# Optimization experiments

Hardware: AMD Instinct MI355X
Metric: run time of the kernel (lower is better)

The kernel has to match this reference:

```python
import jax, jax.numpy as jnp
import numpy as np

N_NODES = 100000
N_EDGES = 1600000
IN_DIM, HID_DIM, OUT_DIM = 128, 256, 512
BN_EPS = 1e-5


def setup_inputs() -> dict:
    key = jax.random.key(0)
    ks = jax.random.split(key, 10)
    x = jax.random.normal(ks[0], (N_NODES, IN_DIM), dtype=jnp.float32)
    edge_index = jax.random.randint(ks[1], (2, N_EDGES), 0, N_NODES, dtype=jnp.int64)
    def lin(k, o, i):
        return jax.random.normal(k, (o, i), dtype=jnp.float32) * (1.0 / np.sqrt(i))
    return {
        "x": x,
        "edge_index": edge_index,
        # SAGEConv 1: in_dim -> hidden_dim (lin_l has bias, lin_r has none)
        "W1l": lin(ks[2], HID_DIM, IN_DIM),
        "b1": jnp.zeros((HID_DIM,), dtype=jnp.float32),
        "W1r": lin(ks[3], HID_DIM, IN_DIM),
        # BatchNorm1d(hidden_dim)
        "gamma": jnp.ones((HID_DIM,), dtype=jnp.float32),
        "beta": jnp.zeros((HID_DIM,), dtype=jnp.float32),
        # SAGEConv 2: hidden_dim -> gnn_out_dim
        "W2l": lin(ks[4], OUT_DIM, HID_DIM),
        "b2": jnp.zeros((OUT_DIM,), dtype=jnp.float32),
        "W2r": lin(ks[5], OUT_DIM, HID_DIM),
    }


def _sage_max(h, src, dst, Wl, b, Wr, n_nodes):
    # gather source features, max-aggregate onto destination nodes
    agg = jax.ops.segment_max(h[src], dst, num_segments=n_nodes)  # [N, D]
    agg = jnp.where(jnp.isneginf(agg), 0.0, agg)  # PyG fills empty segments with 0
    return agg @ Wl.T + b + h @ Wr.T


def reference(x, edge_index, W1l, b1, W1r, gamma, beta, W2l, b2, W2r):
    src, dst = edge_index[0], edge_index[1]
    n = x.shape[0]
    # layer 1: SAGEConv(in_dim, hidden_dim, aggr='max')
    h = _sage_max(x, src, dst, W1l, b1, W1r, n)
    # BatchNorm1d (batch statistics), Dropout is identity in eval; no activation in 'sage' branch
    mean = jnp.mean(h, axis=0)
    var = jnp.var(h, axis=0)
    h = gamma * (h - mean) * jax.lax.rsqrt(var + BN_EPS) + beta
    # layer 2: SAGEConv(hidden_dim, gnn_out_dim, aggr='max')
    out = _sage_max(h, src, dst, W2l, b2, W2r, n)
    return out
```

## Files before the change

### kernel.cpp

```cpp
#include <hip/hip_runtime.h>
#include <hip/hip_bf16.h>
#include <stdint.h>

#define N_NODES 100000
#define N_EDGES 1600000
#define IN_DIM 128
#define HID_DIM 256
#define OUT_DIM 512
#define NBUK 391
#define BCAP 8192
#define EPB 4096

typedef __attribute__((ext_vector_type(4))) float f32x4;
typedef __attribute__((ext_vector_type(8))) short bf16x8;

__device__ __forceinline__ float bf16lo(uint32_t u){ uint32_t b = u << 16; return __builtin_bit_cast(float, b); }
__device__ __forceinline__ float bf16hi(uint32_t u){ uint32_t b = u & 0xffff0000u; return __builtin_bit_cast(float, b); }
__device__ __forceinline__ uint16_t f32_to_bf16(float f){
  uint32_t u = __builtin_bit_cast(uint32_t, f);
  uint32_t r = (u + 0x7fffu + ((u >> 16) & 1u)) >> 16;
  return (uint16_t)r;
}
__device__ __forceinline__ uint32_t pack_bf16_exact(float lo, float hi){
  return (__builtin_bit_cast(uint32_t, hi) & 0xffff0000u) | (__builtin_bit_cast(uint32_t, lo) >> 16);
}
__device__ __forceinline__ uint32_t pack_bf16_rne(float lo, float hi){
  return (uint32_t)f32_to_bf16(lo) | ((uint32_t)f32_to_bf16(hi) << 16);
}
__device__ __forceinline__ void gl2lds16(const void* g, void* l){
  __builtin_amdgcn_global_load_lds(
      (const __attribute__((address_space(1))) uint32_t*)g,
      (__attribute__((address_space(3))) uint32_t*)l, 16, 0, 0);
}

__global__ void k_init(int* __restrict__ gcur, float* __restrict__ sum,
                       float* __restrict__ sumsq){
  int t = threadIdx.x;
  if (t < NBUK) gcur[t] = t << 13;
  if (t < 256){ sum[t] = 0.f; sumsq[t] = 0.f; }
}

__global__ void k_bucket(const int* __restrict__ src, const int* __restrict__ dst,
                         int* __restrict__ gcur, int* __restrict__ ebuk){
  __shared__ int hist[NBUK], curs[NBUK], base[NBUK];
  const int tid = threadIdx.x;
  const int e0 = blockIdx.x * EPB;
  for (int t = tid; t < NBUK; t += 256) hist[t] = 0;
  __syncthreads();
  for (int i = 0; i < EPB; i += 256){
    int e = e0 + i + tid;
    if (e < N_EDGES) atomicAdd(&hist[dst[e] >> 8], 1);
  }
  __syncthreads();
  for (int t = tid; t < NBUK; t += 256){
    int h = hist[t];
    base[t] = h ? atomicAdd(&gcur[t], h) : 0;
    curs[t] = 0;
  }
  __syncthreads();
  for (int i = 0; i < EPB; i += 256){
    int e = e0 + i + tid;
    if (e < N_EDGES){
      int d = dst[e];
      int b = d >> 8;
      int idx = atomicAdd(&curs[b], 1);
      int pos = base[b] + idx;
      if (pos < ((b + 1) << 13))
        ebuk[pos] = ((d & 255) << 17) | src[e];
    }
  }
}

__global__ void k_s2(const int* __restrict__ gcur, int* __restrict__ barr,
                     int* __restrict__ row_start){
  __shared__ int wtot[8];
  const int tid = threadIdx.x, lane = tid & 63, wv = tid >> 6;
  const int val = (tid < NBUK) ? (gcur[tid] - (tid << 13)) : 0;
  int v = val;
  #pragma unroll
  for (int d = 1; d < 64; d <<= 1){ int t = __shfl_up(v, d); if (lane >= d) v += t; }
  if (lane == 63) wtot[wv] = v;
  __syncthreads();
  if (tid < 8){
    int t = wtot[tid];
    #pragma unroll
    for (int d = 1; d < 8; d <<= 1){ int u = __shfl_up(t, d); if (tid >= d) t += u; }
    wtot[tid] = t;
  }
  __syncthreads();
  int excl = (wv ? wtot[wv - 1] : 0) + (v - val);
  if (tid <= NBUK) barr[tid] = excl;
  if (tid == 0) row_start[N_NODES] = N_EDGES;
}

__global__ __launch_bounds__(256)
void k_fillc(const int* __restrict__ gcur, const int* __restrict__ barr,
             const int* __restrict__ ebuk, int* __restrict__ row_start,
             int* __restrict__ esrc){
  __shared__ int ebuf[BCAP];
  __shared__ int cnt[256];
  __shared__ int wtot[4];
  const int b = blockIdx.x, tid = threadIdx.x, lane = tid & 63, wv = tid >> 6;
  const int nodebase = b << 8;
  const int nodecnt = min(256, N_NODES - nodebase);
  int size_b = gcur[b] - (b << 13);
  if (size_b > BCAP) size_b = BCAP;
  const int bs = barr[b];
  cnt[tid] = 0;
  for (int i = tid; i < size_b; i += 256) ebuf[i] = ebuk[(b << 13) + i];
  __syncthreads();
  for (int i = tid; i < size_b; i += 256) atomicAdd(&cnt[ebuf[i] >> 17], 1);
  __syncthreads();
  const int c = cnt[tid];
  int v = c;
  #pragma unroll
  for (int d = 1; d < 64; d <<= 1){ int t = __shfl_up(v, d); if (lane >= d) v += t; }
  if (lane == 63) wtot[wv] = v;
  __syncthreads();
  if (tid < 4){
    int t = wtot[tid];
    #pragma unroll
    for (int d = 1; d < 4; d <<= 1){ int u = __shfl_up(t, d); if (tid >= d) t += u; }
    wtot[tid] = t;
  }
  __syncthreads();
  const int excl = (wv ? wtot[wv - 1] : 0) + (v - c);
  if (tid < nodecnt) row_start[nodebase + tid] = bs + excl;
  cnt[tid] = excl;
  __syncthreads();
  for (int i = tid; i < size_b; i += 256){
    int p = ebuf[i];
    int pos = atomicAdd(&cnt[p >> 17], 1);
    esrc[bs + pos] = p & 0x1FFFF;
  }
}

__global__ void k_convx(const float* __restrict__ x, uint16_t* __restrict__ A1){
  const int idx = blockIdx.x * 256 + threadIdx.x;
  const int n = idx >> 5, q = idx & 31;
  const float4 v = *(const float4*)(x + (long)n * 128 + q * 4);
  ushort4 o;
  o.x = f32_to_bf16(v.x); o.y = f32_to_bf16(v.y);
  o.z = f32_to_bf16(v.z); o.w = f32_to_bf16(v.w);
  *(ushort4*)(A1 + (long)n * 256 + 128 + q * 4) = o;
}

__global__ void k_w1(const float* __restrict__ W1l, const float* __restrict__ W1r,
                     uint16_t* __restrict__ W1cat){
  int idx = blockIdx.x * 256 + threadIdx.x;
  int j = idx >> 8, k = idx & 255;
  float v = (k < 128) ? W1l[j * 128 + k] : W1r[j * 128 + (k - 128)];
  W1cat[idx] = f32_to_bf16(v);
}

__global__ void k_w2(const float* __restrict__ W2l, const float* __restrict__ W2r,
                     const float* __restrict__ b2, const float* __restrict__ scale,
                     const float* __restrict__ shift, uint16_t* __restrict__ W2cat,
                     float* __restrict__ bias2){
  const int wid = (blockIdx.x * 256 + threadIdx.x) >> 6;
  const int lane = threadIdx.x & 63;
  if (wid >= OUT_DIM) return;
  float part = 0.f;
  #pragma unroll
  for (int t = 0; t < 4; t++){
    int k = t * 64 + lane;
    float wl = W2l[(long)wid * 256 + k];
    W2cat[(long)wid * 512 + k] = f32_to_bf16(wl);
    float wr = W2r[(long)wid * 256 + k];
    W2cat[(long)wid * 512 + 256 + k] = f32_to_bf16(wr * scale[k]);
    part += shift[k] * wr;
  }
  #pragma unroll
  for (int d = 32; d > 0; d >>= 1) part += __shfl_xor(part, d);
  if (lane == 0) bias2[wid] = b2[wid] + part;
}

__global__ void k_bncoef(const float* __restrict__ sum, const float* __restrict__ sumsq,
                         const float* __restrict__ gamma, const float* __restrict__ beta,
                         float* __restrict__ scale, float* __restrict__ shift){
  int c = threadIdx.x;
  float inv_n = 1.0f / (float)N_NODES;
  float mean = sum[c] * inv_n;
  float var = sumsq[c] * inv_n - mean * mean;
  float sc = gamma[c] * rsqrtf(var + 1e-5f);
  scale[c] = sc;
  shift[c] = beta[c] - mean * sc;
}

__global__ void k_agg1(const uint32_t* __restrict__ A1u, const int* __restrict__ row_start,
                       const int* __restrict__ esrc, uint32_t* __restrict__ A1w){
  const int wid = (blockIdx.x * 256 + threadIdx.x) >> 6;
  const int lane = threadIdx.x & 63;
  if (wid >= N_NODES) return;
  const int grp = lane >> 4, li = lane & 15;
  const int s0 = row_start[wid], s1 = row_start[wid + 1];
  float m[8];
  #pragma unroll
  for (int j = 0; j < 8; j++) m[j] = -INFINITY;

  #define ACC1(u)                                        \
    m[0] = fmaxf(m[0], bf16lo(u.x)); m[1] = fmaxf(m[1], bf16hi(u.x)); \
    m[2] = fmaxf(m[2], bf16lo(u.y)); m[3] = fmaxf(m[3], bf16hi(u.y)); \
    m[4] = fmaxf(m[4], bf16lo(u.z)); m[5] = fmaxf(m[5], bf16hi(u.z)); \
    m[6] = fmaxf(m[6], bf16lo(u.w)); m[7] = fmaxf(m[7], bf16hi(u.w));

  int e = s0 + grp;
  for (; e + 12 < s1; e += 16){
    const uint4 ua = *(const uint4*)(A1u + (long)esrc[e] * 128 + 64 + li * 4);
    const uint4 ub = *(const uint4*)(A1u + (long)esrc[e + 4] * 128 + 64 + li * 4);
    const uint4 uc = *(const uint4*)(A1u + (long)esrc[e + 8] * 128 + 64 + li * 4);
    const uint4 ud = *(const uint4*)(A1u + (long)esrc[e + 12] * 128 + 64 + li * 4);
    ACC1(ua); ACC1(ub); ACC1(uc); ACC1(ud);
  }
  for (; e < s1; e += 4){
    const uint4 u = *(const uint4*)(A1u + (long)esrc[e] * 128 + 64 + li * 4);
    ACC1(u);
  }
  #undef ACC1
  #pragma unroll
  for (int j = 0; j < 8; j++){
    m[j] = fmaxf(m[j], __shfl_xor(m[j], 16));
    m[j] = fmaxf(m[j], __shfl_xor(m[j], 32));
  }
  if (grp == 0){
    uint4 o;
    if (s1 == s0){ o.x = o.y = o.z = o.w = 0u; }
    else {
      o.x = pack_bf16_exact(m[0], m[1]);
      o.y = pack_bf16_exact(m[2], m[3]);
      o.z = pack_bf16_exact(m[4], m[5]);
      o.w = pack_bf16_exact(m[6], m[7]);
    }
    *(uint4*)(A1w + (long)wid * 128 + li * 4) = o;
  }
}

__global__ void k_agg2(const uint32_t* __restrict__ A2u, const int* __restrict__ row_start,
                       const int* __restrict__ esrc, const float* __restrict__ scale,
                       const float* __restrict__ shift, uint32_t* __restrict__ A2w){
  const int wid = (blockIdx.x * 256 + threadIdx.x) >> 6;
  const int lane = threadIdx.x & 63;
  if (wid >= N_NODES) return;
  const int half = lane >> 5, li = lane & 31;
  const int c0 = li * 8;
  const float4 sca = *(const float4*)(scale + c0);
  const float4 scb = *(const float4*)(scale + c0 + 4);
  const float4 sha = *(const float4*)(shift + c0);
  const float4 shb = *(const float4*)(shift + c0 + 4);
  const int s0 = row_start[wid], s1 = row_start[wid + 1];
  float m[8];
  #pragma unroll
  for (int j = 0; j < 8; j++) m[j] = -INFINITY;

  #define ACC8(u)                                                   \
    m[0] = fmaxf(m[0], fmaf(bf16lo(u.x), sca.x, sha.x));            \
    m[1] = fmaxf(m[1], fmaf(bf16hi(u.x), sca.y, sha.y));            \
    m[2] = fmaxf(m[2], fmaf(bf16lo(u.y), sca.z, sha.z));            \
    m[3] = fmaxf(m[3], fmaf(bf16hi(u.y), sca.w, sha.w));            \
    m[4] = fmaxf(m[4], fmaf(bf16lo(u.z), scb.x, shb.x));            \
    m[5] = fmaxf(m[5], fmaf(bf16hi(u.z), scb.y, shb.y));            \
    m[6] = fmaxf(m[6], fmaf(bf16lo(u.w), scb.z, shb.z));            \
    m[7] = fmaxf(m[7], fmaf(bf16hi(u.w), scb.w, shb.w));

  int e = s0 + half;
  for (; e + 6 < s1; e += 8){
    const uint4 ua = *(const uint4*)(A2u + (long)esrc[e] * 256 + 128 + li * 4);
    const uint4 ub = *(const uint4*)(A2u + (long)esrc[e + 2] * 256 + 128 + li * 4);
    const uint4 uc = *(const uint4*)(A2u + (long)esrc[e + 4] * 256 + 128 + li * 4);
    const uint4 ud = *(const uint4*)(A2u + (long)esrc[e + 6] * 256 + 128 + li * 4);
    ACC8(ua); ACC8(ub); ACC8(uc); ACC8(ud);
  }
  for (; e < s1; e += 2){
    const uint4 u = *(const uint4*)(A2u + (long)esrc[e] * 256 + 128 + li * 4);
    ACC8(u);
  }
  #undef ACC8
  #pragma unroll
  for (int j = 0; j < 8; j++) m[j] = fmaxf(m[j], __shfl_xor(m[j], 32));
  if (half == 0){
    uint4 o;
    if (s1 == s0){ o.x = o.y = o.z = o.w = 0u; }
    else {
      o.x = pack_bf16_rne(m[0], m[1]);
      o.y = pack_bf16_rne(m[2], m[3]);
      o.z = pack_bf16_rne(m[4], m[5]);
      o.w = pack_bf16_rne(m[6], m[7]);
    }
    *(uint4*)(A2w + (long)wid * 256 + li * 4) = o;
  }
}

template<int KT, bool EPI1>
__global__ __launch_bounds__(256, 2)
void k_gemm(const uint16_t* __restrict__ A, const uint16_t* __restrict__ B,
            const float* __restrict__ bias,
            uint16_t* __restrict__ outb, float* __restrict__ outf,
            float* __restrict__ sum, float* __restrict__ sumsq)
{
  constexpr int KB = KT * 2;
  __shared__ uint8_t ldsA[16384];
  __shared__ uint8_t ldsB[16384];
  const int tid = threadIdx.x, lane = tid & 63, wv = tid >> 6;
  const int wvm = wv >> 1, wvn = wv & 1;
  const int mblk = blockIdx.x, nblk = blockIdx.y;

  f32x4 acc[4][4] = {};

  const int srow = wv * 32 + (lane >> 3);
  const int skb  = (lane & 7) * 16;

  const int nsteps = KT / 64;
  for (int ks = 0; ks < nsteps; ++ks){
    #pragma unroll
    for (int i = 0; i < 4; i++){
      int row = srow + i * 8;
      int kbsw = skb ^ ((row & 7) << 4);
      long grow = (long)mblk * 128 + row;
      if (grow > N_NODES - 1) grow = N_NODES - 1;
      gl2lds16((const uint8_t*)A + grow * KB + ks * 128 + kbsw, ldsA + (wv * 4 + i) * 1024);
    }
    #pragma unroll
    for (int i = 0; i < 4; i++){
      int row = srow + i * 8;
      int kbsw = skb ^ ((row & 7) << 4);
      long grow = (long)nblk * 128 + row;
      gl2lds16((const uint8_t*)B + grow * KB + ks * 128 + kbsw, ldsB + (wv * 4 + i) * 1024);
    }
    __syncthreads();

    bf16x8 af[4][2], bfr[4][2];
    #pragma unroll
    for (int m = 0; m < 4; m++){
      int row = wvm * 64 + m * 16 + (lane & 15);
      #pragma unroll
      for (int kk = 0; kk < 2; kk++){
        int kb = kk * 64 + (lane >> 4) * 16;
        af[m][kk] = *(const bf16x8*)(ldsA + row * 128 + (kb ^ ((row & 7) << 4)));
      }
    }
    #pragma unroll
    for (int n = 0; n < 4; n++){
      int row = wvn * 64 + n * 16 + (lane & 15);
      #pragma unroll
      for (int kk = 0; kk < 2; kk++){
        int kb = kk * 64 + (lane >> 4) * 16;
        bfr[n][kk] = *(const bf16x8*)(ldsB + row * 128 + (kb ^ ((row & 7) << 4)));
      }
    }
    #pragma unroll
    for (int kk = 0; kk < 2; kk++)
      #pragma unroll
      for (int m = 0; m < 4; m++)
        #pragma unroll
        for (int n = 0; n < 4; n++)
          acc[m][n] = __builtin_amdgcn_mfma_f32_16x16x32_bf16(af[m][kk], bfr[n][kk], acc[m][n], 0, 0, 0);
    __syncthreads();
  }

  const int rgrp = (lane >> 4) * 4;
  #pragma unroll
  for (int n = 0; n < 4; n++){
    const int col = nblk * 128 + wvn * 64 + n * 16 + (lane & 15);
    const float bv = bias[col];
    float s1v = 0.f, s2v = 0.f;
    #pragma unroll
    for (int m = 0; m < 4; m++){
      const int rowb = mblk * 128 + wvm * 64 + m * 16 + rgrp;
      f32x4 v = acc[m][n];
      #pragma unroll
      for (int j = 0; j < 4; j++){
        const int row = rowb + j;
        const float h = v[j] + bv;
        if (row < N_NODES){
          if (EPI1){
            outb[(long)row * 512 + 256 + col] = f32_to_bf16(h);
            s1v += h; s2v += h * h;
          } else {
            outf[(long)row * 512 + col] = h;
          }
        }
      }
    }
    if (EPI1){
      s1v += __shfl_xor(s1v, 16); s1v += __shfl_xor(s1v, 32);
      s2v += __shfl_xor(s2v, 16); s2v += __shfl_xor(s2v, 32);
      if (lane < 16){
        atomicAdd(&sum[col], s1v);
        atomicAdd(&sumsq[col], s2v);
      }
    }
  }
}

extern "C" void kernel_launch(void* const* d_in, const int* in_sizes, int n_in,
                              void* d_out, int out_size, void* d_ws, size_t ws_size,
                              hipStream_t stream){
  const float* x     = (const float*)d_in[0];
  const int*   ei    = (const int*)d_in[1];
  const float* W1l   = (const float*)d_in[2];
  const float* b1    = (const float*)d_in[3];
  const float* W1r   = (const float*)d_in[4];
  const float* gamma = (const float*)d_in[5];
  const float* beta  = (const float*)d_in[6];
  const float* W2l   = (const float*)d_in[7];
  const float* b2    = (const float*)d_in[8];
  const float* W2r   = (const float*)d_in[9];
  const int* esrc_in = ei;
  const int* edst_in = ei + N_EDGES;

  uint8_t* ws = (uint8_t*)d_ws;
  uint16_t* A1       = (uint16_t*)(ws + 0);
  uint16_t* A2       = (uint16_t*)(ws + 51200000);
  int* ebuk          = (int*)(ws + 51200000);
  int* esrc          = (int*)(ws + 153600000);
  int* row_start     = (int*)(ws + 160000000);
  int* barr          = (int*)(ws + 160400128);
  int* gcur          = (int*)(ws + 160402176);
  uint16_t* W1cat    = (uint16_t*)(ws + 160800256);
  uint16_t* W2cat    = (uint16_t*)(ws + 160931328);
  float* bias2       = (float*)(ws + 161455616);
  float* sum         = (float*)(ws + 161457664);
  float* sumsq       = (float*)(ws + 161458688);
  float* scale       = (float*)(ws + 161459712);
  float* shift       = (float*)(ws + 161460736);

  hipLaunchKernelGGL(k_init, dim3(1), dim3(512), 0, stream, gcur, sum, sumsq);
  hipLaunchKernelGGL(k_bucket, dim3((N_EDGES + EPB - 1) / EPB), dim3(256), 0, stream,
                     esrc_in, edst_in, gcur, ebuk);
  hipLaunchKernelGGL(k_s2, dim3(1), dim3(512), 0, stream, gcur, barr, row_start);
  hipLaunchKernelGGL(k_fillc, dim3(NBUK), dim3(256), 0, stream,
                     gcur, barr, ebuk, row_start, esrc);

  hipLaunchKernelGGL(k_convx, dim3(12500), dim3(256), 0, stream, x, A1);
  hipLaunchKernelGGL(k_w1, dim3(256), dim3(256), 0, stream, W1l, W1r, W1cat);
  hipLaunchKernelGGL(k_agg1, dim3(25000), dim3(256), 0, stream,
                     (const uint32_t*)A1, row_start, esrc, (uint32_t*)A1);

  hipLaunchKernelGGL((k_gemm<256, true>), dim3(782, 2), dim3(256), 0, stream,
                     A1, W1cat, b1, A2, (float*)nullptr, sum, sumsq);

  hipLaunchKernelGGL(k_bncoef, dim3(1), dim3(256), 0, stream, sum, sumsq, gamma, beta, scale, shift);
  hipLaunchKernelGGL(k_w2, dim3(128), dim3(256), 0, stream, W2l, W2r, b2, scale, shift, W2cat, bias2);

  hipLaunchKernelGGL(k_agg2, dim3(25000), dim3(256), 0, stream,
                     (const uint32_t*)A2, row_start, esrc, scale, shift, (uint32_t*)A2);

  hipLaunchKernelGGL((k_gemm<512, false>), dim3(782, 4), dim3(256), 0, stream,
                     A2, W2cat, bias2, (uint16_t*)nullptr, (float*)d_out,
                     (float*)nullptr, (float*)nullptr);
}
```

Before: 461.7 us.

## Double-buffer GEMM LDS loads and fold small setup kernels into neighbours

The GEMM now double-buffers its LDS tiles, prefetching the next K-step while MFMAs run on the current one, and writes the fp32 output with nontemporal stores. Several tiny single-block launches are removed: init is merged into the conversion kernel, the bucket scan is recomputed per block inside the fill kernel, and the BN coefficient computation moves into the weight-prep kernel. The goal is to hide global-to-LDS latency and cut launch overhead. The cost is twice the LDS per block, which can lower occupancy, plus some redundant per-block prefix sums.

```diff
diff --git a/kernel.cpp b/kernel.cpp
--- a/kernel.cpp
+++ b/kernel.cpp
@@ -33,11 +33,22 @@
       (__attribute__((address_space(3))) uint32_t*)l, 16, 0, 0);
 }
 
-__global__ void k_init(int* __restrict__ gcur, float* __restrict__ sum,
-                       float* __restrict__ sumsq){
-  int t = threadIdx.x;
-  if (t < NBUK) gcur[t] = t << 13;
-  if (t < 256){ sum[t] = 0.f; sumsq[t] = 0.f; }
+__global__ void k_convx(const float* __restrict__ x, uint16_t* __restrict__ A1,
+                        int* __restrict__ gcur, float* __restrict__ sum,
+                        float* __restrict__ sumsq){
+  if (blockIdx.x == 12500){
+    const int t = threadIdx.x;
+    for (int i = t; i < NBUK; i += 256) gcur[i] = i << 13;
+    sum[t] = 0.f; sumsq[t] = 0.f;
+    return;
+  }
+  const int idx = blockIdx.x * 256 + threadIdx.x;
+  const int n = idx >> 5, q = idx & 31;
+  const float4 v = *(const float4*)(x + (long)n * 128 + q * 4);
+  ushort4 o;
+  o.x = f32_to_bf16(v.x); o.y = f32_to_bf16(v.y);
+  o.z = f32_to_bf16(v.z); o.w = f32_to_bf16(v.w);
+  *(ushort4*)(A1 + (long)n * 256 + 128 + q * 4) = o;
 }
 
 __global__ void k_bucket(const int* __restrict__ src, const int* __restrict__ dst,
@@ -71,44 +82,27 @@
   }
 }
 
-__global__ void k_s2(const int* __restrict__ gcur, int* __restrict__ barr,
-                     int* __restrict__ row_start){
-  __shared__ int wtot[8];
-  const int tid = threadIdx.x, lane = tid & 63, wv = tid >> 6;
-  const int val = (tid < NBUK) ? (gcur[tid] - (tid << 13)) : 0;
-  int v = val;
-  #pragma unroll
-  for (int d = 1; d < 64; d <<= 1){ int t = __shfl_up(v, d); if (lane >= d) v += t; }
-  if (lane == 63) wtot[wv] = v;
-  __syncthreads();
-  if (tid < 8){
-    int t = wtot[tid];
-    #pragma unroll
-    for (int d = 1; d < 8; d <<= 1){ int u = __shfl_up(t, d); if (tid >= d) t += u; }
-    wtot[tid] = t;
-  }
-  __syncthreads();
-  int excl = (wv ? wtot[wv - 1] : 0) + (v - val);
-  if (tid <= NBUK) barr[tid] = excl;
-  if (tid == 0) row_start[N_NODES] = N_EDGES;
-}
-
 __global__ __launch_bounds__(256)
-void k_fillc(const int* __restrict__ gcur, const int* __restrict__ barr,
-             const int* __restrict__ ebuk, int* __restrict__ row_start,
-             int* __restrict__ esrc){
+void k_fillc(const int* __restrict__ gcur, const int* __restrict__ ebuk,
+             int* __restrict__ row_start, int* __restrict__ esrc){
   __shared__ int ebuf[BCAP];
   __shared__ int cnt[256];
   __shared__ int wtot[4];
+  __shared__ int red[4];
   const int b = blockIdx.x, tid = threadIdx.x, lane = tid & 63, wv = tid >> 6;
   const int nodebase = b << 8;
   const int nodecnt = min(256, N_NODES - nodebase);
+  int accb = 0;
+  for (int t = tid; t < b; t += 256) accb += gcur[t] - (t << 13);
+  #pragma unroll
+  for (int d = 32; d > 0; d >>= 1) accb += __shfl_xor(accb, d);
+  if (lane == 0) red[wv] = accb;
   int size_b = gcur[b] - (b << 13);
   if (size_b > BCAP) size_b = BCAP;
-  const int bs = barr[b];
   cnt[tid] = 0;
   for (int i = tid; i < size_b; i += 256) ebuf[i] = ebuk[(b << 13) + i];
   __syncthreads();
+  const int bs = red[0] + red[1] + red[2] + red[3];
   for (int i = tid; i < size_b; i += 256) atomicAdd(&cnt[ebuf[i] >> 17], 1);
   __syncthreads();
   const int c = cnt[tid];
@@ -126,6 +120,7 @@
   __syncthreads();
   const int excl = (wv ? wtot[wv - 1] : 0) + (v - c);
   if (tid < nodecnt) row_start[nodebase + tid] = bs + excl;
+  if (b == NBUK - 1 && tid == 0) row_start[N_NODES] = N_EDGES;
   cnt[tid] = excl;
   __syncthreads();
   for (int i = tid; i < size_b; i += 256){
@@ -133,16 +128,6 @@
     int pos = atomicAdd(&cnt[p >> 17], 1);
     esrc[bs + pos] = p & 0x1FFFF;
   }
-}
-
-__global__ void k_convx(const float* __restrict__ x, uint16_t* __restrict__ A1){
-  const int idx = blockIdx.x * 256 + threadIdx.x;
-  const int n = idx >> 5, q = idx & 31;
-  const float4 v = *(const float4*)(x + (long)n * 128 + q * 4);
-  ushort4 o;
-  o.x = f32_to_bf16(v.x); o.y = f32_to_bf16(v.y);
-  o.z = f32_to_bf16(v.z); o.w = f32_to_bf16(v.w);
-  *(ushort4*)(A1 + (long)n * 256 + 128 + q * 4) = o;
 }
 
 __global__ void k_w1(const float* __restrict__ W1l, const float* __restrict__ W1r,
@@ -154,12 +139,25 @@
 }
 
 __global__ void k_w2(const float* __restrict__ W2l, const float* __restrict__ W2r,
-                     const float* __restrict__ b2, const float* __restrict__ scale,
-                     const float* __restrict__ shift, uint16_t* __restrict__ W2cat,
-                     float* __restrict__ bias2){
-  const int wid = (blockIdx.x * 256 + threadIdx.x) >> 6;
-  const int lane = threadIdx.x & 63;
-  if (wid >= OUT_DIM) return;
+                     const float* __restrict__ b2, const float* __restrict__ sum,
+                     const float* __restrict__ sumsq, const float* __restrict__ gamma,
+                     const float* __restrict__ beta, uint16_t* __restrict__ W2cat,
+                     float* __restrict__ bias2, float* __restrict__ scale_g,
+                     float* __restrict__ shift_g){
+  __shared__ float sc_s[256], sh_s[256];
+  const int tid = threadIdx.x;
+  {
+    const float inv_n = 1.0f / (float)N_NODES;
+    float mean = sum[tid] * inv_n;
+    float var = sumsq[tid] * inv_n - mean * mean;
+    float sc = gamma[tid] * rsqrtf(var + 1e-5f);
+    float sh = beta[tid] - mean * sc;
+    sc_s[tid] = sc; sh_s[tid] = sh;
+    if (blockIdx.x == 0){ scale_g[tid] = sc; shift_g[tid] = sh; }
+  }
+  __syncthreads();
+  const int wid = (blockIdx.x * 256 + tid) >> 6;
+  const int lane = tid & 63;
   float part = 0.f;
   #pragma unroll
   for (int t = 0; t < 4; t++){
@@ -167,24 +165,12 @@
     float wl = W2l[(long)wid * 256 + k];
     W2cat[(long)wid * 512 + k] = f32_to_bf16(wl);
     float wr = W2r[(long)wid * 256 + k];
-    W2cat[(long)wid * 512 + 256 + k] = f32_to_bf16(wr * scale[k]);
-    part += shift[k] * wr;
+    W2cat[(long)wid * 512 + 256 + k] = f32_to_bf16(wr * sc_s[k]);
+    part += sh_s[k] * wr;
   }
   #pragma unroll
   for (int d = 32; d > 0; d >>= 1) part += __shfl_xor(part, d);
   if (lane == 0) bias2[wid] = b2[wid] + part;
-}
-
-__global__ void k_bncoef(const float* __restrict__ sum, const float* __restrict__ sumsq,
-                         const float* __restrict__ gamma, const float* __restrict__ beta,
-                         float* __restrict__ scale, float* __restrict__ shift){
-  int c = threadIdx.x;
-  float inv_n = 1.0f / (float)N_NODES;
-  float mean = sum[c] * inv_n;
-  float var = sumsq[c] * inv_n - mean * mean;
-  float sc = gamma[c] * rsqrtf(var + 1e-5f);
-  scale[c] = sc;
-  shift[c] = beta[c] - mean * sc;
 }
 
 __global__ void k_agg1(const uint32_t* __restrict__ A1u, const int* __restrict__ row_start,
@@ -279,7 +265,7 @@
   for (int j = 0; j < 8; j++) m[j] = fmaxf(m[j], __shfl_xor(m[j], 32));
   if (half == 0){
     uint4 o;
-    if (s1 == s0){ o.x = o.y = o.z = o.w = 0u; }
+    if (s1 == s0){ o.x = 0u; o.y = 0u; o.z = 0u; o.w = 0u; }
     else {
       o.x = pack_bf16_rne(m[0], m[1]);
       o.y = pack_bf16_rne(m[2], m[3]);
@@ -298,8 +284,8 @@
             float* __restrict__ sum, float* __restrict__ sumsq)
 {
   constexpr int KB = KT * 2;
-  __shared__ uint8_t ldsA[16384];
-  __shared__ uint8_t ldsB[16384];
+  constexpr int NSTEPS = KT / 64;
+  __shared__ uint8_t lds[2][32768];
   const int tid = threadIdx.x, lane = tid & 63, wv = tid >> 6;
   const int wvm = wv >> 1, wvn = wv & 1;
   const int mblk = blockIdx.x, nblk = blockIdx.y;
@@ -309,25 +295,43 @@
   const int srow = wv * 32 + (lane >> 3);
   const int skb  = (lane & 7) * 16;
 
-  const int nsteps = KT / 64;
-  for (int ks = 0; ks < nsteps; ++ks){
-    #pragma unroll
-    for (int i = 0; i < 4; i++){
-      int row = srow + i * 8;
-      int kbsw = skb ^ ((row & 7) << 4);
-      long grow = (long)mblk * 128 + row;
-      if (grow > N_NODES - 1) grow = N_NODES - 1;
-      gl2lds16((const uint8_t*)A + grow * KB + ks * 128 + kbsw, ldsA + (wv * 4 + i) * 1024);
-    }
-    #pragma unroll
-    for (int i = 0; i < 4; i++){
-      int row = srow + i * 8;
-      int kbsw = skb ^ ((row & 7) << 4);
-      long grow = (long)nblk * 128 + row;
-      gl2lds16((const uint8_t*)B + grow * KB + ks * 128 + kbsw, ldsB + (wv * 4 + i) * 1024);
-    }
-    __syncthreads();
-
+  const uint8_t* asrc[4];
+  const uint8_t* bsrc[4];
+  int kbsw_[4];
+  #pragma unroll
+  for (int i = 0; i < 4; i++){
+    int row = srow + i * 8;
+    kbsw_[i] = skb ^ ((row & 7) << 4);
+    long grow = (long)mblk * 128 + row;
+    if (grow > N_NODES - 1) grow = N_NODES - 1;
+    asrc[i] = (const uint8_t*)A + grow * KB + kbsw_[i];
+    bsrc[i] = (const uint8_t*)B + ((long)nblk * 128 + row) * KB + kbsw_[i];
+  }
+
+  #define STAGE(ks, buf)                                              \
+    _Pragma("unroll")                                                 \
+    for (int i = 0; i < 4; i++)                                       \
+      gl2lds16(asrc[i] + (ks) * 128, &lds[buf][(wv * 4 + i) * 1024]); \
+    _Pragma("unroll")                                                 \
+    for (int i = 0; i < 4; i++)                                       \
+      gl2lds16(bsrc[i] + (ks) * 128, &lds[buf][16384 + (wv * 4 + i) * 1024]);
+
+  STAGE(0, 0);
+
+  #pragma unroll
+  for (int ks = 0; ks < NSTEPS; ++ks){
+    const int cur = ks & 1;
+    if (ks + 1 < NSTEPS){
+      STAGE(ks + 1, cur ^ 1);
+      asm volatile("s_waitcnt vmcnt(8)" ::: "memory");
+    } else {
+      asm volatile("s_waitcnt vmcnt(0)" ::: "memory");
+    }
+    __builtin_amdgcn_s_barrier();
+    asm volatile("" ::: "memory");
+
+    const uint8_t* ldsA = &lds[cur][0];
+    const uint8_t* ldsB = &lds[cur][16384];
     bf16x8 af[4][2], bfr[4][2];
     #pragma unroll
     for (int m = 0; m < 4; m++){
@@ -354,8 +358,12 @@
         #pragma unroll
         for (int n = 0; n < 4; n++)
           acc[m][n] = __builtin_amdgcn_mfma_f32_16x16x32_bf16(af[m][kk], bfr[n][kk], acc[m][n], 0, 0, 0);
-    __syncthreads();
-  }
+
+    asm volatile("" ::: "memory");
+    __builtin_amdgcn_s_barrier();
+    asm volatile("" ::: "memory");
+  }
+  #undef STAGE
 
   const int rgrp = (lane >> 4) * 4;
   #pragma unroll
@@ -376,7 +384,7 @@
             outb[(long)row * 512 + 256 + col] = f32_to_bf16(h);
             s1v += h; s2v += h * h;
           } else {
-            outf[(long)row * 512 + col] = h;
+            __builtin_nontemporal_store(h, &outf[(long)row * 512 + col]);
           }
         }
       }
@@ -414,7 +422,6 @@
   int* ebuk          = (int*)(ws + 51200000);
   int* esrc          = (int*)(ws + 153600000);
   int* row_start     = (int*)(ws + 160000000);
-  int* barr          = (int*)(ws + 160400128);
   int* gcur          = (int*)(ws + 160402176);
   uint16_t* W1cat    = (uint16_t*)(ws + 160800256);
   uint16_t* W2cat    = (uint16_t*)(ws + 160931328);
@@ -424,14 +431,12 @@
   float* scale       = (float*)(ws + 161459712);
   float* shift       = (float*)(ws + 161460736);
 
-  hipLaunchKernelGGL(k_init, dim3(1), dim3(512), 0, stream, gcur, sum, sumsq);
+  hipLaunchKernelGGL(k_convx, dim3(12501), dim3(256), 0, stream, x, A1, gcur, sum, sumsq);
   hipLaunchKernelGGL(k_bucket, dim3((N_EDGES + EPB - 1) / EPB), dim3(256), 0, stream,
                      esrc_in, edst_in, gcur, ebuk);
-  hipLaunchKernelGGL(k_s2, dim3(1), dim3(512), 0, stream, gcur, barr, row_start);
   hipLaunchKernelGGL(k_fillc, dim3(NBUK), dim3(256), 0, stream,
-                     gcur, barr, ebuk, row_start, esrc);
-
-  hipLaunchKernelGGL(k_convx, dim3(12500), dim3(256), 0, stream, x, A1);
+                     gcur, ebuk, row_start, esrc);
+
   hipLaunchKernelGGL(k_w1, dim3(256), dim3(256), 0, stream, W1l, W1r, W1cat);
   hipLaunchKernelGGL(k_agg1, dim3(25000), dim3(256), 0, stream,
                      (const uint32_t*)A1, row_start, esrc, (uint32_t*)A1);
@@ -439,8 +444,8 @@
   hipLaunchKernelGGL((k_gemm<256, true>), dim3(782, 2), dim3(256), 0, stream,
                      A1, W1cat, b1, A2, (float*)nullptr, sum, sumsq);
 
-  hipLaunchKernelGGL(k_bncoef, dim3(1), dim3(256), 0, stream, sum, sumsq, gamma, beta, scale, shift);
-  hipLaunchKernelGGL(k_w2, dim3(128), dim3(256), 0, stream, W2l, W2r, b2, scale, shift, W2cat, bias2);
+  hipLaunchKernelGGL(k_w2, dim3(128), dim3(256), 0, stream,
+                     W2l, W2r, b2, sum, sumsq, gamma, beta, W2cat, bias2, scale, shift);
 
   hipLaunchKernelGGL(k_agg2, dim3(25000), dim3(256), 0, stream,
                      (const uint32_t*)A2, row_start, esrc, scale, shift, (uint32_t*)A2);
```

Measured after the change: 438.3 us. -5.1%, faster.
